# Kernel tuning notes

Measured on AMD Instinct MI355X. Metric: run time of the kernel, lower is better.

## Reference

```python
import jax, jax.numpy as jnp
import numpy as np

N_NODES = 50000
N_EDGES = 800000
IN_DIM, HID_DIM, OUT_DIM = 128, 96, 40


def setup_inputs() -> dict:
    key = jax.random.key(0)
    ks = jax.random.split(key, 8)
    x = jax.random.normal(ks[0], (N_NODES, IN_DIM), dtype=jnp.float32)
    edge_src = jax.random.randint(ks[1], (N_EDGES,), 0, N_NODES, dtype=jnp.int32)
    edge_dst = jax.random.randint(ks[2], (N_EDGES,), 0, N_NODES, dtype=jnp.int32)
    edge_val = jax.random.uniform(ks[3], (N_EDGES,), dtype=jnp.float32)
    W1 = jax.random.normal(ks[4], (IN_DIM, HID_DIM), dtype=jnp.float32) * 0.05
    b1 = jax.random.normal(ks[5], (HID_DIM,), dtype=jnp.float32) * 0.05
    W2 = jax.random.normal(ks[6], (HID_DIM, OUT_DIM), dtype=jnp.float32) * 0.05
    b2 = jax.random.normal(ks[7], (OUT_DIM,), dtype=jnp.float32) * 0.05
    return {"x": x, "edge_val": edge_val, "W1": W1, "b1": b1,
            "W2": W2, "b2": b2, "edge_src": edge_src, "edge_dst": edge_dst}


def _spmm(edge_src, edge_dst, edge_val, dense, num_nodes):
    # out[i] = sum_{e: dst[e]==i} val[e] * dense[src[e]]  (COO sparse @ dense)
    msgs = edge_val[:, None] * dense[edge_src]  # [E, D]
    return jax.ops.segment_sum(msgs, edge_dst, num_segments=num_nodes)


def reference(x, edge_val, W1, b1, W2, b2, edge_src, edge_dst):
    n = x.shape[0]
    # GraphConv 1: support = x @ W1; out = A @ support + b1
    h = _spmm(edge_src, edge_dst, edge_val, x @ W1, n) + b1
    h = jax.nn.relu(h)  # dropout is identity in eval mode
    # GraphConv 2
    out = _spmm(edge_src, edge_dst, edge_val, h @ W2, n) + b2
    return jax.nn.log_softmax(out, axis=1)
```

## Files before the change

kernel.cpp:

```cpp
#include <hip/hip_runtime.h>
#include <hip/hip_fp16.h>
#include <math.h>

#define N_NODES 50000
#define N_EDGES 800000
#define IN_DIM 128
#define HID_DIM 96
#define OUT_DIM 40
#define CAP 48

typedef __attribute__((ext_vector_type(8))) unsigned short ushort8_t;

static __device__ __forceinline__ unsigned short f2bf(float f) {
    unsigned int u = __float_as_uint(f);
    u += 0x7FFFu + ((u >> 16) & 1u);
    return (unsigned short)(u >> 16);
}
static __device__ __forceinline__ float bf2f(unsigned short h) {
    return __uint_as_float(((unsigned int)h) << 16);
}

__global__ __launch_bounds__(256) void fill_kernel(
    const int* __restrict__ esrc, const int* __restrict__ edst,
    const float* __restrict__ eval, int* __restrict__ cnt,
    unsigned int* __restrict__ recs) {
    int e = blockIdx.x * 256 + threadIdx.x;
    if (e >= N_EDGES) return;
    int d = edst[e];
    int pos = atomicAdd(&cnt[d], 1);
    if (pos < CAP) {
        unsigned int rec = (unsigned int)esrc[e] |
            ((unsigned int)__half_as_ushort(__float2half(eval[e])) << 16);
        recs[(size_t)d * CAP + pos] = rec;
    }
}

__global__ __launch_bounds__(256) void gemm1_kernel(
    const float* __restrict__ x, const float* __restrict__ W1,
    unsigned short* __restrict__ supb, int n) {
    __shared__ float sX[64][IN_DIM / 2 + 4];
    __shared__ float sW[64][HID_DIM];
    const int t = threadIdx.x;
    const int row0 = blockIdx.x * 64;
    const int tx = t & 15;
    const int rg = t >> 4;

    float acc[4][6] = {};

    for (int kc = 0; kc < 2; ++kc) {
        for (int i = t; i < 64 * 16; i += 256) {
            int r = i >> 4;
            int c4 = i & 15;
            int gr = row0 + r;
            float4 v = make_float4(0.f, 0.f, 0.f, 0.f);
            if (gr < n) v = ((const float4*)x)[gr * (IN_DIM / 4) + kc * 16 + c4];
            ((float4*)&sX[r][0])[c4] = v;
        }
        for (int i = t; i < 64 * 24; i += 256) {
            int kr = i / 24;
            int c4 = i % 24;
            ((float4*)&sW[kr][0])[c4] = ((const float4*)W1)[(kc * 64 + kr) * 24 + c4];
        }
        __syncthreads();
        #pragma unroll 8
        for (int k = 0; k < 64; ++k) {
            float xv[4];
            #pragma unroll
            for (int i = 0; i < 4; ++i) xv[i] = sX[rg * 4 + i][k];
            #pragma unroll
            for (int j = 0; j < 6; ++j) {
                float wv = sW[k][tx + 16 * j];
                #pragma unroll
                for (int i = 0; i < 4; ++i) acc[i][j] += xv[i] * wv;
            }
        }
        __syncthreads();
    }
    #pragma unroll
    for (int i = 0; i < 4; ++i) {
        int gr = row0 + rg * 4 + i;
        if (gr < n) {
            #pragma unroll
            for (int j = 0; j < 6; ++j)
                supb[gr * HID_DIM + tx + 16 * j] = f2bf(acc[i][j]);
        }
    }
}

__global__ __launch_bounds__(256) void gather1_gemm2_kernel(
    const unsigned short* __restrict__ supb, const unsigned int* __restrict__ recs,
    const int* __restrict__ cnt, const float* __restrict__ b1,
    const float* __restrict__ W2, unsigned short* __restrict__ yb) {
    __shared__ float sH[21][HID_DIM + 4];
    __shared__ float sW2[HID_DIM * OUT_DIM];
    __shared__ unsigned int sRec[21][52];
    const int t = threadIdx.x;
    const int dst0 = blockIdx.x * 21;
    const int g = t / 12, l = t % 12;
    const int dst = dst0 + g;
    const bool active = (t < 252) && (dst < N_NODES);

    for (int i = t; i < HID_DIM * OUT_DIM / 4; i += 256)
        ((float4*)sW2)[i] = ((const float4*)W2)[i];

    for (int i = t; i < 21 * 12; i += 256) {
        int gg = i / 12, q = i % 12;
        int dd = dst0 + gg;
        if (dd < N_NODES)
            ((uint4*)&sRec[gg][0])[q] = ((const uint4*)(recs + (size_t)dd * CAP))[q];
    }
    __syncthreads();

    if (active) {
        int deg = cnt[dst];
        deg = deg < CAP ? deg : CAP;
        float acc[8] = {};
        const int c8 = l;
        for (int p = 0; p < deg; ++p) {
            unsigned int r = sRec[g][p];
            int s = (int)(r & 0xFFFFu);
            float v = __half2float(__ushort_as_half((unsigned short)(r >> 16)));
            ushort8_t sv = ((const ushort8_t*)(supb + (size_t)s * HID_DIM))[c8];
            #pragma unroll
            for (int j = 0; j < 8; ++j) acc[j] += v * bf2f(sv[j]);
        }
        float4 r0, r1;
        r0.x = fmaxf(acc[0] + b1[c8 * 8 + 0], 0.f);
        r0.y = fmaxf(acc[1] + b1[c8 * 8 + 1], 0.f);
        r0.z = fmaxf(acc[2] + b1[c8 * 8 + 2], 0.f);
        r0.w = fmaxf(acc[3] + b1[c8 * 8 + 3], 0.f);
        r1.x = fmaxf(acc[4] + b1[c8 * 8 + 4], 0.f);
        r1.y = fmaxf(acc[5] + b1[c8 * 8 + 5], 0.f);
        r1.z = fmaxf(acc[6] + b1[c8 * 8 + 6], 0.f);
        r1.w = fmaxf(acc[7] + b1[c8 * 8 + 7], 0.f);
        float4* hp = (float4*)&sH[g][c8 * 8];
        hp[0] = r0;
        hp[1] = r1;
    }
    __syncthreads();

    for (int idx = t; idx < 21 * OUT_DIM; idx += 256) {
        int d = idx / OUT_DIM, c = idx % OUT_DIM;
        int dd = dst0 + d;
        if (dd >= N_NODES) continue;
        const float4* hr = (const float4*)&sH[d][0];
        float s = 0.f;
        #pragma unroll
        for (int k4 = 0; k4 < HID_DIM / 4; ++k4) {
            float4 hv = hr[k4];
            s += hv.x * sW2[(k4 * 4 + 0) * OUT_DIM + c]
               + hv.y * sW2[(k4 * 4 + 1) * OUT_DIM + c]
               + hv.z * sW2[(k4 * 4 + 2) * OUT_DIM + c]
               + hv.w * sW2[(k4 * 4 + 3) * OUT_DIM + c];
        }
        yb[(size_t)dd * OUT_DIM + c] = f2bf(s);
    }
}

__global__ __launch_bounds__(256) void gather2_lsm_kernel(
    const unsigned short* __restrict__ yb, const unsigned int* __restrict__ recs,
    const int* __restrict__ cnt, const float* __restrict__ b2,
    float* __restrict__ out) {
    __shared__ unsigned int sRec[50][52];
    __shared__ float part[256];
    __shared__ float smax[50];
    __shared__ float ssum[50];
    const int t = threadIdx.x;
    const int g = t / 5;
    const int c8 = t % 5;
    int dst = blockIdx.x * 50 + g;
    bool active = (t < 250) && (dst < N_NODES);

    for (int i = t; i < 50 * 12; i += 256) {
        int gg = i / 12, q = i % 12;
        int dd = blockIdx.x * 50 + gg;
        if (dd < N_NODES)
            ((uint4*)&sRec[gg][0])[q] = ((const uint4*)(recs + (size_t)dd * CAP))[q];
    }
    __syncthreads();

    float acc[8] = {};
    if (active) {
        int deg = cnt[dst];
        deg = deg < CAP ? deg : CAP;
        for (int p = 0; p < deg; ++p) {
            unsigned int r = sRec[g][p];
            int s = (int)(r & 0xFFFFu);
            float v = __half2float(__ushort_as_half((unsigned short)(r >> 16)));
            ushort8_t sv = ((const ushort8_t*)(yb + (size_t)s * OUT_DIM))[c8];
            #pragma unroll
            for (int j = 0; j < 8; ++j) acc[j] += v * bf2f(sv[j]);
        }
        #pragma unroll
        for (int j = 0; j < 8; ++j) acc[j] += b2[c8 * 8 + j];
    }
    float lmax = -INFINITY;
    #pragma unroll
    for (int j = 0; j < 8; ++j) lmax = fmaxf(lmax, acc[j]);
    part[t] = active ? lmax : -INFINITY;
    __syncthreads();
    if (t < 50) {
        float m = part[t * 5];
        #pragma unroll
        for (int i = 1; i < 5; ++i) m = fmaxf(m, part[t * 5 + i]);
        smax[t] = m;
    }
    __syncthreads();
    float m = active ? smax[g] : 0.f;
    float lsum = 0.f;
    #pragma unroll
    for (int j = 0; j < 8; ++j) lsum += expf(acc[j] - m);
    part[t] = active ? lsum : 0.f;
    __syncthreads();
    if (t < 50) {
        float s = 0.f;
        #pragma unroll
        for (int i = 0; i < 5; ++i) s += part[t * 5 + i];
        ssum[t] = logf(s);
    }
    __syncthreads();
    if (active) {
        float ls = ssum[g];
        float* op = out + (size_t)dst * OUT_DIM + c8 * 8;
        ((float4*)op)[0] = make_float4(acc[0] - m - ls, acc[1] - m - ls,
                                       acc[2] - m - ls, acc[3] - m - ls);
        ((float4*)op)[1] = make_float4(acc[4] - m - ls, acc[5] - m - ls,
                                       acc[6] - m - ls, acc[7] - m - ls);
    }
}

extern "C" void kernel_launch(void* const* d_in, const int* in_sizes, int n_in,
                              void* d_out, int out_size, void* d_ws, size_t ws_size,
                              hipStream_t stream) {
    const float* x        = (const float*)d_in[0];
    const float* edge_val = (const float*)d_in[1];
    const float* W1       = (const float*)d_in[2];
    const float* b1       = (const float*)d_in[3];
    const float* W2       = (const float*)d_in[4];
    const float* b2       = (const float*)d_in[5];
    const int*   esrc     = (const int*)d_in[6];
    const int*   edst     = (const int*)d_in[7];
    float* out = (float*)d_out;

    int*   cnt  = (int*)d_ws;
    unsigned int* recs = (unsigned int*)(cnt + 50048);
    unsigned short* supb = (unsigned short*)(recs + (size_t)N_NODES * CAP);
    unsigned short* yb   = supb + (size_t)N_NODES * HID_DIM;

    hipMemsetAsync(cnt, 0, N_NODES * sizeof(int), stream);
    fill_kernel<<<(N_EDGES + 255) / 256, 256, 0, stream>>>(
        esrc, edst, edge_val, cnt, recs);
    gemm1_kernel<<<(N_NODES + 63) / 64, 256, 0, stream>>>(x, W1, supb, N_NODES);
    gather1_gemm2_kernel<<<(N_NODES + 20) / 21, 256, 0, stream>>>(
        supb, recs, cnt, b1, W2, yb);
    gather2_lsm_kernel<<<(N_NODES + 49) / 50, 256, 0, stream>>>(
        yb, recs, cnt, b2, out);
}
```

Baseline: 211.3 us.

## Restructure gemm1 to keep full W1 in LDS and stream x rows from global

gemm1 now loads all of W1 into shared memory once per block and has each thread read float4 chunks of x for 8 rows directly from global memory into registers. The x tile no longer goes through shared memory, and each block covers 128 rows instead of 64 with an 8x6 register tile per thread. This removes the staged x loads into LDS and the two sync phases, and raises arithmetic per W load. In exchange it uses more registers and 48KB of LDS per block, and the per-thread x loads are strided by row, so they may coalesce poorly and lower occupancy.

```diff
diff --git a/kernel.cpp b/kernel.cpp
--- a/kernel.cpp
+++ b/kernel.cpp
@@ -38,47 +38,46 @@
 __global__ __launch_bounds__(256) void gemm1_kernel(
     const float* __restrict__ x, const float* __restrict__ W1,
     unsigned short* __restrict__ supb, int n) {
-    __shared__ float sX[64][IN_DIM / 2 + 4];
-    __shared__ float sW[64][HID_DIM];
+    __shared__ float sW[IN_DIM * HID_DIM];
     const int t = threadIdx.x;
-    const int row0 = blockIdx.x * 64;
+    const int row0 = blockIdx.x * 128;
     const int tx = t & 15;
     const int rg = t >> 4;
 
-    float acc[4][6] = {};
-
-    for (int kc = 0; kc < 2; ++kc) {
-        for (int i = t; i < 64 * 16; i += 256) {
-            int r = i >> 4;
-            int c4 = i & 15;
-            int gr = row0 + r;
-            float4 v = make_float4(0.f, 0.f, 0.f, 0.f);
-            if (gr < n) v = ((const float4*)x)[gr * (IN_DIM / 4) + kc * 16 + c4];
-            ((float4*)&sX[r][0])[c4] = v;
-        }
-        for (int i = t; i < 64 * 24; i += 256) {
-            int kr = i / 24;
-            int c4 = i % 24;
-            ((float4*)&sW[kr][0])[c4] = ((const float4*)W1)[(kc * 64 + kr) * 24 + c4];
-        }
-        __syncthreads();
-        #pragma unroll 8
-        for (int k = 0; k < 64; ++k) {
-            float xv[4];
-            #pragma unroll
-            for (int i = 0; i < 4; ++i) xv[i] = sX[rg * 4 + i][k];
-            #pragma unroll
-            for (int j = 0; j < 6; ++j) {
-                float wv = sW[k][tx + 16 * j];
+    #pragma unroll
+    for (int i = 0; i < 12; ++i)
+        ((float4*)sW)[t + 256 * i] = ((const float4*)W1)[t + 256 * i];
+    __syncthreads();
+
+    float acc[8][6] = {};
+    const int r0 = row0 + rg * 8;
+
+    for (int k4 = 0; k4 < IN_DIM / 4; ++k4) {
+        float4 xv[8];
+        #pragma unroll
+        for (int i = 0; i < 8; ++i) {
+            int gr = r0 + i;
+            xv[i] = (gr < n) ? ((const float4*)x)[gr * (IN_DIM / 4) + k4]
+                             : make_float4(0.f, 0.f, 0.f, 0.f);
+        }
+        #pragma unroll
+        for (int kk = 0; kk < 4; ++kk) {
+            const float* wr = sW + (k4 * 4 + kk) * HID_DIM + tx;
+            float wv[6];
+            #pragma unroll
+            for (int j = 0; j < 6; ++j) wv[j] = wr[16 * j];
+            #pragma unroll
+            for (int i = 0; i < 8; ++i) {
+                float xs = (kk == 0) ? xv[i].x : (kk == 1) ? xv[i].y
+                         : (kk == 2) ? xv[i].z : xv[i].w;
                 #pragma unroll
-                for (int i = 0; i < 4; ++i) acc[i][j] += xv[i] * wv;
+                for (int j = 0; j < 6; ++j) acc[i][j] += xs * wv[j];
             }
         }
-        __syncthreads();
-    }
-    #pragma unroll
-    for (int i = 0; i < 4; ++i) {
-        int gr = row0 + rg * 4 + i;
+    }
+    #pragma unroll
+    for (int i = 0; i < 8; ++i) {
+        int gr = r0 + i;
         if (gr < n) {
             #pragma unroll
             for (int j = 0; j < 6; ++j)
@@ -250,7 +249,7 @@
     hipMemsetAsync(cnt, 0, N_NODES * sizeof(int), stream);
     fill_kernel<<<(N_EDGES + 255) / 256, 256, 0, stream>>>(
         esrc, edst, edge_val, cnt, recs);
-    gemm1_kernel<<<(N_NODES + 63) / 64, 256, 0, stream>>>(x, W1, supb, N_NODES);
+    gemm1_kernel<<<(N_NODES + 127) / 128, 256, 0, stream>>>(x, W1, supb, N_NODES);
     gather1_gemm2_kernel<<<(N_NODES + 20) / 21, 256, 0, stream>>>(
         supb, recs, cnt, b1, W2, yb);
     gather2_lsm_kernel<<<(N_NODES + 49) / 50, 256, 0, stream>>>(
```

After: 234.8 us. 1.11x slower.
